# Kernel optimization log

Hardware: AMD Instinct MI355X
Metric: run time of the kernel (lower is better)

The kernel has to match this reference:

```python
import jax, jax.numpy as jnp
import numpy as np

B = 32768      # batch
D = 2          # input_dim
H = 2048       # hidden_dim
NQ = 4         # qubits


def setup_inputs() -> dict:
    key = jax.random.key(0)
    ks = jax.random.split(key, 14)

    def lin(k, fan_in, fan_out):
        # kaiming-uniform-ish init like nn.Linear
        bound = 1.0 / np.sqrt(fan_in)
        kw, kb = jax.random.split(k)
        W = jax.random.uniform(kw, (fan_in, fan_out), jnp.float32, -bound, bound)
        b = jax.random.uniform(kb, (fan_out,), jnp.float32, -bound, bound)
        return W, b

    x = jax.random.normal(ks[0], (B, D), jnp.float32)
    W1, b1 = lin(ks[1], D + NQ, H)      # core Linear 1
    W2, b2 = lin(ks[2], H, H)           # core Linear 2
    Wc, bc = lin(ks[3], H, 1)           # classifier
    Wr1, br1 = lin(ks[4], D, 8)
    Wr2, br2 = lin(ks[5], 8, 4)
    Wr3, br3 = lin(ks[6], 4, 1)
    return dict(x=x, W1=W1, b1=b1, W2=W2, b2=b2, Wc=Wc, bc=bc,
                Wr1=Wr1, br1=br1, Wr2=Wr2, br2=br2, Wr3=Wr3, br3=br3)


def _quantum_feature_map(x):
    # Exact closed form of: RY(x_i) on 4 qubits from |0000>, CNOT(0,1), CNOT(2,3),
    # expval(PauliZ(i)). Padding with zeros -> cos(0)=1 on unused wires.
    xq = jnp.pad(x, ((0, 0), (0, NQ - x.shape[1])))  # [B,4]
    c = jnp.cos(xq)
    return jnp.stack([c[:, 0], c[:, 0] * c[:, 1], c[:, 2], c[:, 2] * c[:, 3]], axis=1)


def reference(x, W1, b1, W2, b2, Wc, bc, Wr1, br1, Wr2, br2, Wr3, br3):
    qfeat = _quantum_feature_map(x)               # [B,4]
    concat = jnp.concatenate([x, qfeat], axis=1)  # [B, D+4]
    h = jnp.tanh(concat @ W1 + b1)                # [B,H]
    h = jnp.tanh(h @ W2 + b2)                     # [B,H]
    logits = h @ Wc + bc                          # [B,1]
    r = jnp.tanh(x @ Wr1 + br1)
    r = jnp.tanh(r @ Wr2 + br2)
    risk = r @ Wr3 + br3                          # [B,1]
    return logits, risk
```

## Files before the change

kernel.cpp:

```cpp
#include <hip/hip_runtime.h>
#include <hip/hip_bf16.h>
#include <stdint.h>

#define B_ROWS 32768
#define HID    2048
#define K_DIM  2048

#define BT  128
#define BKB 128

#define SCALE_W   5747.3639f
#define DEQUANT   1.3700225e-6f

#define L1_BLOCKS (B_ROWS / 32)
#define TR_BLOCKS ((HID/32)*(K_DIM/32))

typedef int  int4v __attribute__((ext_vector_type(4)));
typedef char char8 __attribute__((ext_vector_type(8)));

__device__ __forceinline__ float fast_tanh(float x) {
    float e = __expf(2.0f * x);
    return 1.0f - 2.0f * __builtin_amdgcn_rcpf(e + 1.0f);
}

__device__ __forceinline__ void gl_lds16(const void* g, void* l) {
    __builtin_amdgcn_global_load_lds(
        (const __attribute__((address_space(1))) void*)(uintptr_t)g,
        (__attribute__((address_space(3))) void*)(uint32_t)(uintptr_t)l,
        16, 0, 0);
}

__global__ __launch_bounds__(256) void prep_kernel(
    const float* __restrict__ x,   const float* __restrict__ W1, const float* __restrict__ b1,
    const float* __restrict__ W2,
    const float* __restrict__ Wr1, const float* __restrict__ br1,
    const float* __restrict__ Wr2, const float* __restrict__ br2,
    const float* __restrict__ Wr3, const float* __restrict__ br3,
    const float* __restrict__ bc,
    char* __restrict__ h1, char* __restrict__ W2t, float* __restrict__ out) {
    const int t = threadIdx.x;
    if (blockIdx.x >= L1_BLOCKS) {
        __shared__ float tile[32][33];
        const int tb = blockIdx.x - L1_BLOCKS;
        const int n0 = (tb & 63) * 32;
        const int k0 = (tb >> 6) * 32;
        const int tx = t & 31;
        const int ty = t >> 5;
#pragma unroll
        for (int i = 0; i < 4; ++i) {
            int k = k0 + ty + i * 8;
            tile[ty + i * 8][tx] = W2[(size_t)k * HID + n0 + tx];
        }
        __syncthreads();
#pragma unroll
        for (int i = 0; i < 4; ++i) {
            int n = n0 + ty + i * 8;
            W2t[(size_t)n * K_DIM + k0 + tx] =
                (char)__float2int_rn(tile[tx][ty + i * 8] * SCALE_W);
        }
        return;
    }
    const int n0 = t * 8;
    float w0[8], w1[8], w2[8], w3[8], wb[8];
#pragma unroll
    for (int j = 0; j < 8; ++j) {
        w0[j] = W1[0 * HID + n0 + j];
        w1[j] = W1[1 * HID + n0 + j];
        w2[j] = W1[2 * HID + n0 + j];
        w3[j] = W1[3 * HID + n0 + j];
        wb[j] = W1[4 * HID + n0 + j] + W1[5 * HID + n0 + j] + b1[n0 + j];
    }
    const int brow0 = blockIdx.x * 32;
    for (int r = 0; r < 32; ++r) {
        const int b = brow0 + r;
        const float x0 = x[2 * b], x1 = x[2 * b + 1];
        const float c0 = cosf(x0);
        const float cc = c0 * cosf(x1);
        char8 v;
#pragma unroll
        for (int j = 0; j < 8; ++j) {
            float z = wb[j] + x0 * w0[j] + x1 * w1[j] + c0 * w2[j] + cc * w3[j];
            v[j] = (char)__float2int_rn(fast_tanh(z) * 127.0f);
        }
        *(char8*)(h1 + (size_t)b * HID + n0) = v;
    }
    if (t < 32) {
        const int b = brow0 + t;
        const float x0 = x[2 * b], x1 = x[2 * b + 1];
        float r1[8];
#pragma unroll
        for (int j = 0; j < 8; ++j)
            r1[j] = fast_tanh(br1[j] + x0 * Wr1[j] + x1 * Wr1[8 + j]);
        float r2[4];
#pragma unroll
        for (int j = 0; j < 4; ++j) {
            float s = br2[j];
#pragma unroll
            for (int i = 0; i < 8; ++i) s += r1[i] * Wr2[i * 4 + j];
            r2[j] = fast_tanh(s);
        }
        float risk = br3[0];
#pragma unroll
        for (int i = 0; i < 4; ++i) risk += r2[i] * Wr3[i];
        out[B_ROWS + b] = risk;
        out[b]          = bc[0];
    }
}

__global__ __launch_bounds__(128, 2) void gemm_kernel(
    const char* __restrict__ A,
    const char* __restrict__ Bt,
    const float* __restrict__ b2, const float* __restrict__ Wc,
    float* __restrict__ out) {
    __shared__ __align__(16) char sA[BT * BKB];
    __shared__ __align__(16) char sB[BT * BKB];

    const int tid  = threadIdx.x;
    const int wave = tid >> 6;
    const int lane = tid & 63;
    const int bid  = blockIdx.x;
    const int m0 = (bid >> 4) * BT;
    const int n0 = (bid & 15) * BT;

    const char* aSrc[8]; char* aDst[8];
    const char* bSrc[8]; char* bDst[8];
    {
        const int rsub  = lane >> 3;
        const int chunk = (lane & 7) ^ rsub;
#pragma unroll
        for (int i = 0; i < 8; ++i) {
            int seg = wave * 8 + i;
            aSrc[i] = A + (size_t)(m0 + seg * 8 + rsub) * K_DIM + chunk * 16;
            aDst[i] = sA + seg * 1024;
            bSrc[i] = Bt + (size_t)(n0 + seg * 8 + rsub) * K_DIM + chunk * 16;
            bDst[i] = sB + seg * 1024;
        }
    }

    int4v acc[4][8] = {};
    const int mw   = wave * 64;
    const int quad = lane >> 4;
    const int r16  = lane & 15;
    const int x7   = lane & 7;

    for (int kb = 0; kb < K_DIM / BKB; ++kb) {
#pragma unroll
        for (int i = 0; i < 8; ++i) {
            gl_lds16(aSrc[i], aDst[i]);  aSrc[i] += BKB;
            gl_lds16(bSrc[i], bDst[i]);  bSrc[i] += BKB;
        }
        __syncthreads();
#pragma unroll
        for (int ks = 0; ks < 2; ++ks) {
            const int slot = ((ks * 4 + quad) ^ x7) * 16;
            int4v af[4], bfr[8];
#pragma unroll
            for (int mi = 0; mi < 4; ++mi)
                af[mi]  = *(const int4v*)(sA + (mw + mi * 16 + r16) * BKB + slot);
#pragma unroll
            for (int ni = 0; ni < 8; ++ni)
                bfr[ni] = *(const int4v*)(sB + (ni * 16 + r16) * BKB + slot);
#pragma unroll
            for (int mi = 0; mi < 4; ++mi)
#pragma unroll
                for (int ni = 0; ni < 8; ++ni)
                    acc[mi][ni] = __builtin_amdgcn_mfma_i32_16x16x64_i8(
                        af[mi], bfr[ni], acc[mi][ni], 0, 0, 0);
        }
        __syncthreads();
    }

    float b2v[8], wcv[8];
#pragma unroll
    for (int ni = 0; ni < 8; ++ni) {
        int gn = n0 + ni * 16 + r16;
        b2v[ni] = b2[gn];
        wcv[ni] = Wc[gn];
    }
#pragma unroll
    for (int mi = 0; mi < 4; ++mi) {
#pragma unroll
        for (int r = 0; r < 4; ++r) {
            int gm = m0 + mw + mi * 16 + quad * 4 + r;
            float rs = 0.f;
#pragma unroll
            for (int ni = 0; ni < 8; ++ni)
                rs += fast_tanh((float)acc[mi][ni][r] * DEQUANT + b2v[ni]) * wcv[ni];
            rs += __shfl_xor(rs, 1);
            rs += __shfl_xor(rs, 2);
            rs += __shfl_xor(rs, 4);
            rs += __shfl_xor(rs, 8);
            if (r16 == 0) atomicAdd(&out[gm], rs);
        }
    }
}

extern "C" void kernel_launch(void* const* d_in, const int* in_sizes, int n_in,
                              void* d_out, int out_size, void* d_ws, size_t ws_size,
                              hipStream_t stream) {
    const float* x   = (const float*)d_in[0];
    const float* W1  = (const float*)d_in[1];
    const float* b1  = (const float*)d_in[2];
    const float* W2  = (const float*)d_in[3];
    const float* b2  = (const float*)d_in[4];
    const float* Wc  = (const float*)d_in[5];
    const float* bc  = (const float*)d_in[6];
    const float* Wr1 = (const float*)d_in[7];
    const float* br1 = (const float*)d_in[8];
    const float* Wr2 = (const float*)d_in[9];
    const float* br2 = (const float*)d_in[10];
    const float* Wr3 = (const float*)d_in[11];
    const float* br3 = (const float*)d_in[12];
    float* out = (float*)d_out;

    char* W2t = (char*)d_ws;
    char* h1  = (char*)d_ws + (size_t)4 * 1024 * 1024;

    prep_kernel<<<L1_BLOCKS + TR_BLOCKS, 256, 0, stream>>>(
        x, W1, b1, W2, Wr1, br1, Wr2, br2, Wr3, br3, bc, h1, W2t, out);
    gemm_kernel<<<(B_ROWS / BT) * (HID / BT), 128, 0, stream>>>(h1, W2t, b2, Wc, out);
}
```

Before: 277.9 us.

## Store h1 in MFMA-fragment layout and load A directly from global

```diff
diff --git a/kernel.cpp b/kernel.cpp
--- a/kernel.cpp
+++ b/kernel.cpp
@@ -6,8 +6,10 @@
 #define HID    2048
 #define K_DIM  2048
 
-#define BT  128
+#define BM 128
+#define BN 256
 #define BKB 128
+#define NWIN (K_DIM / BKB)
 
 #define SCALE_W   5747.3639f
 #define DEQUANT   1.3700225e-6f
@@ -15,8 +17,8 @@
 #define L1_BLOCKS (B_ROWS / 32)
 #define TR_BLOCKS ((HID/32)*(K_DIM/32))
 
-typedef int  int4v __attribute__((ext_vector_type(4)));
-typedef char char8 __attribute__((ext_vector_type(8)));
+typedef int  int4v  __attribute__((ext_vector_type(4)));
+typedef char char16 __attribute__((ext_vector_type(16)));
 
 __device__ __forceinline__ float fast_tanh(float x) {
     float e = __expf(2.0f * x);
@@ -29,6 +31,7 @@
         (__attribute__((address_space(3))) void*)(uint32_t)(uintptr_t)l,
         16, 0, 0);
 }
+
 
 __global__ __launch_bounds__(256) void prep_kernel(
     const float* __restrict__ x,   const float* __restrict__ W1, const float* __restrict__ b1,
@@ -37,7 +40,7 @@
     const float* __restrict__ Wr2, const float* __restrict__ br2,
     const float* __restrict__ Wr3, const float* __restrict__ br3,
     const float* __restrict__ bc,
-    char* __restrict__ h1, char* __restrict__ W2t, float* __restrict__ out) {
+    char* __restrict__ h1t, char* __restrict__ W2t, float* __restrict__ out) {
     const int t = threadIdx.x;
     if (blockIdx.x >= L1_BLOCKS) {
         __shared__ float tile[32][33];
@@ -60,10 +63,12 @@
         }
         return;
     }
-    const int n0 = t * 8;
-    float w0[8], w1[8], w2[8], w3[8], wb[8];
-#pragma unroll
-    for (int j = 0; j < 8; ++j) {
+    const int tx = t & 127;
+    const int ty = t >> 7;
+    const int n0 = tx * 16;
+    float w0[16], w1[16], w2[16], w3[16], wb[16];
+#pragma unroll
+    for (int j = 0; j < 16; ++j) {
         w0[j] = W1[0 * HID + n0 + j];
         w1[j] = W1[1 * HID + n0 + j];
         w2[j] = W1[2 * HID + n0 + j];
@@ -71,18 +76,20 @@
         wb[j] = W1[4 * HID + n0 + j] + W1[5 * HID + n0 + j] + b1[n0 + j];
     }
     const int brow0 = blockIdx.x * 32;
-    for (int r = 0; r < 32; ++r) {
+    char* base = h1t + (size_t)(brow0 >> 4) * 32768
+               + (n0 >> 6) * 1024 + ((n0 >> 4) & 3) * 256;
+    for (int r = ty; r < 32; r += 2) {
         const int b = brow0 + r;
         const float x0 = x[2 * b], x1 = x[2 * b + 1];
         const float c0 = cosf(x0);
         const float cc = c0 * cosf(x1);
-        char8 v;
-#pragma unroll
-        for (int j = 0; j < 8; ++j) {
+        char16 v;
+#pragma unroll
+        for (int j = 0; j < 16; ++j) {
             float z = wb[j] + x0 * w0[j] + x1 * w1[j] + c0 * w2[j] + cc * w3[j];
             v[j] = (char)__float2int_rn(fast_tanh(z) * 127.0f);
         }
-        *(char8*)(h1 + (size_t)b * HID + n0) = v;
+        *(char16*)(base + (r >> 4) * 32768 + (r & 15) * 16) = v;
     }
     if (t < 32) {
         const int b = brow0 + t;
@@ -107,22 +114,20 @@
     }
 }
 
-__global__ __launch_bounds__(128, 2) void gemm_kernel(
-    const char* __restrict__ A,
+__global__ __launch_bounds__(256, 2) void gemm_kernel(
+    const char* __restrict__ At,
     const char* __restrict__ Bt,
     const float* __restrict__ b2, const float* __restrict__ Wc,
     float* __restrict__ out) {
-    __shared__ __align__(16) char sA[BT * BKB];
-    __shared__ __align__(16) char sB[BT * BKB];
+    __shared__ __align__(16) char sB[BN * BKB];
 
     const int tid  = threadIdx.x;
     const int wave = tid >> 6;
     const int lane = tid & 63;
     const int bid  = blockIdx.x;
-    const int m0 = (bid >> 4) * BT;
-    const int n0 = (bid & 15) * BT;
-
-    const char* aSrc[8]; char* aDst[8];
+    const int m0 = (bid >> 3) * BM;
+    const int n0 = (bid & 7) * BN;
+
     const char* bSrc[8]; char* bDst[8];
     {
         const int rsub  = lane >> 3;
@@ -130,36 +135,40 @@
 #pragma unroll
         for (int i = 0; i < 8; ++i) {
             int seg = wave * 8 + i;
-            aSrc[i] = A + (size_t)(m0 + seg * 8 + rsub) * K_DIM + chunk * 16;
-            aDst[i] = sA + seg * 1024;
             bSrc[i] = Bt + (size_t)(n0 + seg * 8 + rsub) * K_DIM + chunk * 16;
             bDst[i] = sB + seg * 1024;
         }
     }
 
     int4v acc[4][8] = {};
-    const int mw   = wave * 64;
+    const int mw   = (wave & 1) * 64;
+    const int nw   = (wave >> 1) * 128;
     const int quad = lane >> 4;
     const int r16  = lane & 15;
     const int x7   = lane & 7;
 
-    for (int kb = 0; kb < K_DIM / BKB; ++kb) {
+    const char* aP[4];
+#pragma unroll
+    for (int mi = 0; mi < 4; ++mi)
+        aP[mi] = At + (size_t)((m0 + mw) >> 4 << 15) + mi * 32768 + lane * 16;
+
+    for (int w = 0; w < NWIN; ++w) {
 #pragma unroll
         for (int i = 0; i < 8; ++i) {
-            gl_lds16(aSrc[i], aDst[i]);  aSrc[i] += BKB;
-            gl_lds16(bSrc[i], bDst[i]);  bSrc[i] += BKB;
+            gl_lds16(bSrc[i], bDst[i]);
+            bSrc[i] += BKB;
         }
         __syncthreads();
 #pragma unroll
         for (int ks = 0; ks < 2; ++ks) {
+            int4v af[4], bfr[8];
+#pragma unroll
+            for (int mi = 0; mi < 4; ++mi)
+                af[mi] = *(const int4v*)(aP[mi] + ks * 1024);
             const int slot = ((ks * 4 + quad) ^ x7) * 16;
-            int4v af[4], bfr[8];
-#pragma unroll
-            for (int mi = 0; mi < 4; ++mi)
-                af[mi]  = *(const int4v*)(sA + (mw + mi * 16 + r16) * BKB + slot);
 #pragma unroll
             for (int ni = 0; ni < 8; ++ni)
-                bfr[ni] = *(const int4v*)(sB + (ni * 16 + r16) * BKB + slot);
+                bfr[ni] = *(const int4v*)(sB + (nw + ni * 16 + r16) * BKB + slot);
 #pragma unroll
             for (int mi = 0; mi < 4; ++mi)
 #pragma unroll
@@ -167,13 +176,15 @@
                     acc[mi][ni] = __builtin_amdgcn_mfma_i32_16x16x64_i8(
                         af[mi], bfr[ni], acc[mi][ni], 0, 0, 0);
         }
+#pragma unroll
+        for (int mi = 0; mi < 4; ++mi) aP[mi] += 2048;
         __syncthreads();
     }
 
     float b2v[8], wcv[8];
 #pragma unroll
     for (int ni = 0; ni < 8; ++ni) {
-        int gn = n0 + ni * 16 + r16;
+        int gn = n0 + nw + ni * 16 + r16;
         b2v[ni] = b2[gn];
         wcv[ni] = Wc[gn];
     }
@@ -214,9 +225,9 @@
     float* out = (float*)d_out;
 
     char* W2t = (char*)d_ws;
-    char* h1  = (char*)d_ws + (size_t)4 * 1024 * 1024;
+    char* h1t = (char*)d_ws + (size_t)4 * 1024 * 1024;
 
     prep_kernel<<<L1_BLOCKS + TR_BLOCKS, 256, 0, stream>>>(
-        x, W1, b1, W2, Wr1, br1, Wr2, br2, Wr3, br3, bc, h1, W2t, out);
-    gemm_kernel<<<(B_ROWS / BT) * (HID / BT), 128, 0, stream>>>(h1, W2t, b2, Wc, out);
-}
+        x, W1, b1, W2, Wr1, br1, Wr2, br2, Wr3, br3, bc, h1t, W2t, out);
+    gemm_kernel<<<(B_ROWS / BM) * (HID / BN), 256, 0, stream>>>(h1t, W2t, b2, Wc, out);
+}
```

After: 299.6 us. +7.8%, slower.

## Warp-specialize int8 GEMM with producer waves and double-buffered LDS

Applied to the files above, without the earlier changes.

```diff
diff --git a/kernel.cpp b/kernel.cpp
--- a/kernel.cpp
+++ b/kernel.cpp
@@ -8,6 +8,8 @@
 
 #define BT  128
 #define BKB 128
+#define NWIN (K_DIM / BKB)
+#define STAGE 32768
 
 #define SCALE_W   5747.3639f
 #define DEQUANT   1.3700225e-6f
@@ -107,13 +109,12 @@
     }
 }
 
-__global__ __launch_bounds__(128, 2) void gemm_kernel(
+__global__ __launch_bounds__(256, 2) void gemm_kernel(
     const char* __restrict__ A,
     const char* __restrict__ Bt,
     const float* __restrict__ b2, const float* __restrict__ Wc,
     float* __restrict__ out) {
-    __shared__ __align__(16) char sA[BT * BKB];
-    __shared__ __align__(16) char sB[BT * BKB];
+    __shared__ __align__(16) char lds[2][STAGE];
 
     const int tid  = threadIdx.x;
     const int wave = tid >> 6;
@@ -122,53 +123,76 @@
     const int m0 = (bid >> 4) * BT;
     const int n0 = (bid & 15) * BT;
 
-    const char* aSrc[8]; char* aDst[8];
-    const char* bSrc[8]; char* bDst[8];
-    {
+    const bool producer = wave >= 2;
+
+    const char* src[16]; int dst[16];
+    if (producer) {
+        const int pw    = wave - 2;
         const int rsub  = lane >> 3;
         const int chunk = (lane & 7) ^ rsub;
 #pragma unroll
         for (int i = 0; i < 8; ++i) {
-            int seg = wave * 8 + i;
-            aSrc[i] = A + (size_t)(m0 + seg * 8 + rsub) * K_DIM + chunk * 16;
-            aDst[i] = sA + seg * 1024;
-            bSrc[i] = Bt + (size_t)(n0 + seg * 8 + rsub) * K_DIM + chunk * 16;
-            bDst[i] = sB + seg * 1024;
+            int seg = pw * 8 + i;
+            src[i] = A + (size_t)(m0 + seg * 8 + rsub) * K_DIM + chunk * 16;
+            dst[i] = seg * 1024;
+        }
+#pragma unroll
+        for (int i = 0; i < 8; ++i) {
+            int seg = pw * 8 + i;
+            src[8 + i] = Bt + (size_t)(n0 + seg * 8 + rsub) * K_DIM + chunk * 16;
+            dst[8 + i] = 16384 + seg * 1024;
+        }
+#pragma unroll
+        for (int i = 0; i < 16; ++i) {
+            gl_lds16(src[i], &lds[0][dst[i]]);
+            src[i] += BKB;
         }
     }
 
     int4v acc[4][8] = {};
-    const int mw   = wave * 64;
+    const int mw   = (wave & 1) * 64;
     const int quad = lane >> 4;
     const int r16  = lane & 15;
     const int x7   = lane & 7;
 
-    for (int kb = 0; kb < K_DIM / BKB; ++kb) {
-#pragma unroll
-        for (int i = 0; i < 8; ++i) {
-            gl_lds16(aSrc[i], aDst[i]);  aSrc[i] += BKB;
-            gl_lds16(bSrc[i], bDst[i]);  bSrc[i] += BKB;
+    __syncthreads();
+
+#pragma unroll 1
+    for (int w = 0; w < NWIN; ++w) {
+        if (producer) {
+            if (w + 1 < NWIN) {
+                char* buf = lds[(w + 1) & 1];
+#pragma unroll
+                for (int i = 0; i < 16; ++i) {
+                    gl_lds16(src[i], buf + dst[i]);
+                    src[i] += BKB;
+                }
+            }
+        } else {
+            const char* sA = lds[w & 1];
+            const char* sB = sA + 16384;
+#pragma unroll
+            for (int ks = 0; ks < 2; ++ks) {
+                const int slot = ((ks * 4 + quad) ^ x7) * 16;
+                int4v af[4], bfr[8];
+#pragma unroll
+                for (int mi = 0; mi < 4; ++mi)
+                    af[mi]  = *(const int4v*)(sA + (mw + mi * 16 + r16) * BKB + slot);
+#pragma unroll
+                for (int ni = 0; ni < 8; ++ni)
+                    bfr[ni] = *(const int4v*)(sB + (ni * 16 + r16) * BKB + slot);
+#pragma unroll
+                for (int mi = 0; mi < 4; ++mi)
+#pragma unroll
+                    for (int ni = 0; ni < 8; ++ni)
+                        acc[mi][ni] = __builtin_amdgcn_mfma_i32_16x16x64_i8(
+                            af[mi], bfr[ni], acc[mi][ni], 0, 0, 0);
+            }
         }
         __syncthreads();
-#pragma unroll
-        for (int ks = 0; ks < 2; ++ks) {
-            const int slot = ((ks * 4 + quad) ^ x7) * 16;
-            int4v af[4], bfr[8];
-#pragma unroll
-            for (int mi = 0; mi < 4; ++mi)
-                af[mi]  = *(const int4v*)(sA + (mw + mi * 16 + r16) * BKB + slot);
-#pragma unroll
-            for (int ni = 0; ni < 8; ++ni)
-                bfr[ni] = *(const int4v*)(sB + (ni * 16 + r16) * BKB + slot);
-#pragma unroll
-            for (int mi = 0; mi < 4; ++mi)
-#pragma unroll
-                for (int ni = 0; ni < 8; ++ni)
-                    acc[mi][ni] = __builtin_amdgcn_mfma_i32_16x16x64_i8(
-                        af[mi], bfr[ni], acc[mi][ni], 0, 0, 0);
-        }
-        __syncthreads();
-    }
+    }
+
+    if (producer) return;
 
     float b2v[8], wcv[8];
 #pragma unroll
@@ -218,5 +242,5 @@
 
     prep_kernel<<<L1_BLOCKS + TR_BLOCKS, 256, 0, stream>>>(
         x, W1, b1, W2, Wr1, br1, Wr2, br2, Wr3, br3, bc, h1, W2t, out);
-    gemm_kernel<<<(B_ROWS / BT) * (HID / BT), 128, 0, stream>>>(h1, W2t, b2, Wc, out);
-}
+    gemm_kernel<<<(B_ROWS / BT) * (HID / BT), 256, 0, stream>>>(h1, W2t, b2, Wc, out);
+}
```

New measurement: 301.1 us. 1.08x slower.
